# Kernel tuning notes

Measured on AMD Instinct MI355X. Metric: run time of the kernel, lower is better.

Reference implementation:

```python
import jax, jax.numpy as jnp
import numpy as np

DT = 1.0
COLL_COEF = 0.5  # module in training mode
TWO_PI = 2.0 * np.pi


def safe_norm_ch(d):
    # L2 norm over channel axis (axis=1) with torch-like zero-safe gradient
    sq = jnp.sum(d * d, axis=1)
    nz = sq > 0
    return jnp.sqrt(jnp.where(nz, sq, 1.0)) * nz


def setup_inputs() -> dict:
    key = jax.random.key(0)
    k1, k2, k3, k4 = jax.random.split(key, 4)
    bs, C, X = 4, 256, 1024
    kinet_dim = 128
    n = kinet_dim  # n_divide = max_channal // C = 1
    P = n * (n - 1) // 2  # 8128
    return {
        "x": jax.random.normal(k1, (bs, C, X), jnp.float32),
        "v": jax.random.normal(k2, (bs, C, X), jnp.float32),
        "a": jax.random.normal(k3, (bs, C, X), jnp.float32),
        "rand_u": jax.random.uniform(k4, (bs, C, P), jnp.float32),
        "collision_dims": jnp.arange(kinet_dim, dtype=jnp.int32),
    }


def reference(x, v, a, rand_u, collision_dims):
    dims = collision_dims
    xs = x[:, :, dims]          # (bs, chnl, n)  (n_divide == 1, view is a no-op)
    as_ = a[:, :, dims]
    bs, chnl, n = xs.shape
    vv = as_ * DT               # code overwrites v with a*dt
    xx = xs

    # pairwise relative / center-of-mass quantities
    x_r = safe_norm_ch(xx[:, :, :, None] - xx[:, :, None, :])       # (bs, n, n)
    v_r = safe_norm_ch(vv[:, :, :, None] - vv[:, :, None, :])       # (bs, n, n)
    v_cm = (vv[:, :, :, None] + vv[:, :, None, :]) * 0.5            # (bs, chnl, n, n)
    x_cm = (xx[:, :, :, None] + xx[:, :, None, :]) * 0.5            # (bs, chnl, n, n)

    u_x = jnp.exp(-x_r)
    v_r_max = jnp.max(v_r, axis=(1, 2), keepdims=True)              # (bs, 1, 1)
    mask = v_r / v_r_max * u_x
    collision_mask = mask > (1.0 - COLL_COEF)                       # (bs, n, n) bool

    # antisymmetric projection of the upper triangle of v_r
    iu, ju = np.triu_indices(n, k=1)
    rand_vec = TWO_PI * rand_u                                      # (bs, chnl, P)
    proj = v_r[:, iu, ju][:, None, :] * rand_vec                    # (bs, chnl, P)
    vrl = jnp.zeros((bs, chnl, n, n), xs.dtype)
    vrl = vrl.at[:, :, iu, ju].set(proj)
    vrl = vrl.at[:, :, ju, iu].set(-proj)

    delta_v = v_cm + vrl - vv[:, :, :, None]                        # (bs, chnl, n, n)
    cmask = collision_mask[:, None, :, :]
    v_new = vv + jnp.sum(delta_v * cmask, axis=2)                   # (bs, chnl, n)

    cm = collision_mask.astype(xs.dtype) + jnp.eye(n, dtype=xs.dtype)[None]
    x_new = jnp.sum(x_cm * cm[:, None], axis=2) / jnp.sum(cm, axis=2)[:, None, :]
    x_new = x_new + v_new * (DT / 2.0)

    # reassemble: zero collision dims of x and a, add, write back updated coords
    out = x.at[:, :, dims].set(0.0) + a.at[:, :, dims].set(0.0)
    out = out.at[:, :, dims].set(x_new.reshape(bs, chnl, n))
    return out
```

## Files before the change

### kernel.cpp

```cpp
#include <hip/hip_runtime.h>
#include <math.h>

#define BS 4
#define CH 256
#define XD 1024
#define N 128
#define NP 8128
#define TWO_PI_F 6.283185307179586f
#define PADU 132

typedef __fp16 h2v __attribute__((ext_vector_type(2)));

__device__ __forceinline__ h2v u2h(unsigned u) {
  union { unsigned u; h2v h; } x; x.u = u; return x.h;
}
__device__ __forceinline__ unsigned h2u(h2v h) {
  union { unsigned u; h2v h; } x; x.h = h; return x.u;
}

__global__ __launch_bounds__(256) void k1_pair_pass(
    const float* __restrict__ x, const float* __restrict__ a,
    const int* __restrict__ dims,
    float* __restrict__ vrS, float* __restrict__ mS,
    float* __restrict__ pmaxV, float* __restrict__ pmaxM,
    float* __restrict__ out) {
  int ti = blockIdx.x, tj = blockIdx.y, b = blockIdx.z;
  int t = threadIdx.x;
  __shared__ unsigned sXi[16][PADU], sXj[16][PADU], sAi[16][PADU], sAj[16][PADU];
  __shared__ unsigned inset[XD / 32];
  __shared__ float wred[16];

  if (t < XD / 32) inset[t] = 0u;
  __syncthreads();
  int d16 = t & 15, grp = t >> 4;
  int di, dj;
  if (t < N) atomicOr(&inset[dims[t] >> 5], 1u << (dims[t] & 31));
  di = dims[ti * 16 + d16];
  dj = dims[tj * 16 + d16];
  __syncthreads();

  {
    int B = (b << 6) + (tj << 3) + ti;
    int row = (B << 2) + (t >> 6);
    int q0 = t & 63;
    const float4* x4 = (const float4*)(x + (size_t)row * XD);
    const float4* a4 = (const float4*)(a + (size_t)row * XD);
    float4* o4 = (float4*)(out + (size_t)row * XD);
#pragma unroll
    for (int q = 0; q < 4; ++q) {
      int e = q0 + (q << 6);
      unsigned nib = (inset[e >> 3] >> ((e & 7) * 4)) & 0xFu;
      float4 xv = x4[e], av = a4[e];
      float4 o;
      o.x = fmaf((nib & 1u) ? 0.5f : 1.0f, av.x, xv.x);
      o.y = fmaf((nib & 2u) ? 0.5f : 1.0f, av.y, xv.y);
      o.z = fmaf((nib & 4u) ? 0.5f : 1.0f, av.z, xv.z);
      o.w = fmaf((nib & 8u) ? 0.5f : 1.0f, av.w, xv.w);
      o4[e] = o;
    }
  }

  {
    const float* xb = x + (size_t)b * CH * XD;
    const float* ab = a + (size_t)b * CH * XD;
    int c0 = grp * 16;
#pragma unroll
    for (int s = 0; s < 4; ++s) {
      const float* src = (s & 1) ? ab : xb;
      int d = (s & 2) ? dj : di;
      unsigned pk[8];
#pragma unroll
      for (int k = 0; k < 8; ++k) {
        float f0 = src[(size_t)(c0 + 2 * k) * XD + d];
        float f1 = src[(size_t)(c0 + 2 * k + 1) * XD + d];
        pk[k] = h2u(__builtin_amdgcn_cvt_pkrtz(f0, f1));
      }
      unsigned* dst = (s & 2) ? ((s & 1) ? &sAj[d16][0] : &sXj[d16][0])
                              : ((s & 1) ? &sAi[d16][0] : &sXi[d16][0]);
      *(uint4*)&dst[grp * 8] = make_uint4(pk[0], pk[1], pk[2], pk[3]);
      *(uint4*)&dst[grp * 8 + 4] = make_uint4(pk[4], pk[5], pk[6], pk[7]);
    }
  }
  __syncthreads();

  int ii = t >> 4, jj = t & 15;
  float accx = 0.f, accv = 0.f;
#pragma unroll 8
  for (int cq = 0; cq < 32; ++cq) {
    uint4 xi = *(const uint4*)&sXi[ii][cq * 4];
    uint4 xj = *(const uint4*)&sXj[jj][cq * 4];
    uint4 ai = *(const uint4*)&sAi[ii][cq * 4];
    uint4 aj = *(const uint4*)&sAj[jj][cq * 4];
    h2v d0 = u2h(xi.x) - u2h(xj.x);
    accx = __builtin_amdgcn_fdot2(d0, d0, accx, false);
    h2v d1 = u2h(xi.y) - u2h(xj.y);
    accx = __builtin_amdgcn_fdot2(d1, d1, accx, false);
    h2v d2 = u2h(xi.z) - u2h(xj.z);
    accx = __builtin_amdgcn_fdot2(d2, d2, accx, false);
    h2v d3 = u2h(xi.w) - u2h(xj.w);
    accx = __builtin_amdgcn_fdot2(d3, d3, accx, false);
    h2v e0 = u2h(ai.x) - u2h(aj.x);
    accv = __builtin_amdgcn_fdot2(e0, e0, accv, false);
    h2v e1 = u2h(ai.y) - u2h(aj.y);
    accv = __builtin_amdgcn_fdot2(e1, e1, accv, false);
    h2v e2 = u2h(ai.z) - u2h(aj.z);
    accv = __builtin_amdgcn_fdot2(e2, e2, accv, false);
    h2v e3 = u2h(ai.w) - u2h(aj.w);
    accv = __builtin_amdgcn_fdot2(e3, e3, accv, false);
  }
  float vr = sqrtf(accv);
  float mv = vr * expf(-sqrtf(accx));
  int i = ti * 16 + ii, j = tj * 16 + jj;
  vrS[((size_t)b * N + i) * N + j] = vr;
  mS[((size_t)b * N + i) * N + j] = mv;

  float wv = vr, wm = mv;
#pragma unroll
  for (int off = 32; off; off >>= 1) {
    wv = fmaxf(wv, __shfl_xor(wv, off));
    wm = fmaxf(wm, __shfl_xor(wm, off));
  }
  int wid = t >> 6;
  if ((t & 63) == 0) { wred[wid] = wv; wred[8 + wid] = wm; }
  __syncthreads();
  if (t == 0) {
    int tile = (b << 6) + (ti << 3) + tj;
    pmaxV[tile] = fmaxf(fmaxf(wred[0], wred[1]), fmaxf(wred[2], wred[3]));
    pmaxM[tile] = fmaxf(fmaxf(wred[8], wred[9]), fmaxf(wred[10], wred[11]));
  }
}

__global__ __launch_bounds__(256) void k2_fixup(
    const float* __restrict__ x, const float* __restrict__ a,
    const float* __restrict__ ru, const int* __restrict__ dims,
    const float* __restrict__ vrS, const float* __restrict__ mS,
    const float* __restrict__ pmaxV, const float* __restrict__ pmaxM,
    float* __restrict__ out) {
  int cg = blockIdx.x, b = blockIdx.y;
  int t = threadIdx.x;
  __shared__ float mx2[2];
  __shared__ float xx[N], vv[N];
  __shared__ int dsh[N];

  if (t < 64) {
    float pv = pmaxV[(b << 6) + t];
    float pm = pmaxM[(b << 6) + t];
#pragma unroll
    for (int off = 32; off; off >>= 1) {
      pv = fmaxf(pv, __shfl_xor(pv, off));
      pm = fmaxf(pm, __shfl_xor(pm, off));
    }
    if (t == 0) { mx2[0] = pv; mx2[1] = pm; }
  }
  __syncthreads();
  float vrmax = mx2[0], mmax = mx2[1];
  float inv = vrmax > 0.f ? 1.f / vrmax : 0.f;
  if (!(mmax * inv > 0.5f)) return;

  if (t < N) dsh[t] = dims[t];
  for (int cc = 0; cc < 32; ++cc) {
    int c = (cg << 5) + cc;
    int bc = (b << 8) + c;
    __syncthreads();
    if (t < N) {
      int d = dsh[t];
      xx[t] = x[(size_t)bc * XD + d];
      vv[t] = a[(size_t)bc * XD + d];
    }
    __syncthreads();
    if (t < N) {
      int j = t;
      const float* mcol = mS + (size_t)b * N * N + j;
      const float* vcol = vrS + (size_t)b * N * N + j;
      const float* rub = ru + (size_t)bc * NP;
      float S = 0.f, sumV = 0.f, sumX = 0.f, R = 0.f;
      for (int i = 0; i < N; ++i) {
        float mv = mcol[(size_t)i * N];
        if (mv * inv > 0.5f) {
          S += 1.f;
          sumV += vv[i];
          sumX += xx[i];
          float vrv = vcol[(size_t)i * N];
          int p;
          float sgn;
          if (i < j) {
            p = i * N - ((i * (i + 1)) >> 1) + (j - i - 1);
            sgn = 1.f;
          } else {
            p = j * N - ((j * (j + 1)) >> 1) + (i - j - 1);
            sgn = -1.f;
          }
          R += sgn * TWO_PI_F * vrv * rub[p];
        }
      }
      float vj = vv[j];
      float v_new = vj + 0.5f * S * vj - 0.5f * sumV + R;
      float x_new = 0.5f * xx[j] + 0.5f * (xx[j] + sumX) / (S + 1.f) + 0.5f * v_new;
      out[(size_t)bc * XD + dsh[j]] = x_new;
    }
  }
}

extern "C" void kernel_launch(void* const* d_in, const int* in_sizes, int n_in,
                              void* d_out, int out_size, void* d_ws, size_t ws_size,
                              hipStream_t stream) {
  const float* x = (const float*)d_in[0];
  const float* a = (const float*)d_in[2];
  const float* ru = (const float*)d_in[3];
  const int* dims = (const int*)d_in[4];
  float* out = (float*)d_out;

  float* vrS = (float*)d_ws;
  float* mS = vrS + (size_t)BS * N * N;
  float* pmaxV = mS + (size_t)BS * N * N;
  float* pmaxM = pmaxV + BS * 64;

  k1_pair_pass<<<dim3(8, 8, BS), 256, 0, stream>>>(x, a, dims, vrS, mS, pmaxV,
                                                   pmaxM, out);
  k2_fixup<<<dim3(8, BS), 256, 0, stream>>>(x, a, ru, dims, vrS, mS, pmaxV,
                                            pmaxM, out);
}
```

Measured before the change: 12.80 us.

## Widen pair-pass blocks to 1024 threads with split-channel partial sums

Each pair-pass block grows from 256 to 1024 threads. The streaming copy, the strided gather of the four channel tiles, and the channel dot-product loop are each split four ways across the extra threads. The channel partial sums are reduced through new shared-memory arrays before the sqrt/exp and max reduction, which adds a barrier. The aim is more memory-level parallelism and latency hiding for a small 256-block grid, at the cost of more shared memory and synchronisation per block.

```diff
diff --git a/kernel.cpp b/kernel.cpp
--- a/kernel.cpp
+++ b/kernel.cpp
@@ -18,7 +18,7 @@
   union { unsigned u; h2v h; } x; x.h = h; return x.u;
 }
 
-__global__ __launch_bounds__(256) void k1_pair_pass(
+__global__ __launch_bounds__(1024, 4) void k1_pair_pass(
     const float* __restrict__ x, const float* __restrict__ a,
     const int* __restrict__ dims,
     float* __restrict__ vrS, float* __restrict__ mS,
@@ -27,101 +27,105 @@
   int ti = blockIdx.x, tj = blockIdx.y, b = blockIdx.z;
   int t = threadIdx.x;
   __shared__ unsigned sXi[16][PADU], sXj[16][PADU], sAi[16][PADU], sAj[16][PADU];
+  __shared__ float paccX[4][256], paccV[4][256];
   __shared__ unsigned inset[XD / 32];
   __shared__ float wred[16];
 
   if (t < XD / 32) inset[t] = 0u;
   __syncthreads();
-  int d16 = t & 15, grp = t >> 4;
-  int di, dj;
   if (t < N) atomicOr(&inset[dims[t] >> 5], 1u << (dims[t] & 31));
-  di = dims[ti * 16 + d16];
-  dj = dims[tj * 16 + d16];
   __syncthreads();
 
   {
     int B = (b << 6) + (tj << 3) + ti;
-    int row = (B << 2) + (t >> 6);
-    int q0 = t & 63;
+    int row = (B << 2) + (t >> 8);
+    int e = t & 255;
     const float4* x4 = (const float4*)(x + (size_t)row * XD);
     const float4* a4 = (const float4*)(a + (size_t)row * XD);
     float4* o4 = (float4*)(out + (size_t)row * XD);
-#pragma unroll
-    for (int q = 0; q < 4; ++q) {
-      int e = q0 + (q << 6);
-      unsigned nib = (inset[e >> 3] >> ((e & 7) * 4)) & 0xFu;
-      float4 xv = x4[e], av = a4[e];
-      float4 o;
-      o.x = fmaf((nib & 1u) ? 0.5f : 1.0f, av.x, xv.x);
-      o.y = fmaf((nib & 2u) ? 0.5f : 1.0f, av.y, xv.y);
-      o.z = fmaf((nib & 4u) ? 0.5f : 1.0f, av.z, xv.z);
-      o.w = fmaf((nib & 8u) ? 0.5f : 1.0f, av.w, xv.w);
-      o4[e] = o;
-    }
+    unsigned nib = (inset[e >> 3] >> ((e & 7) * 4)) & 0xFu;
+    float4 xv = x4[e], av = a4[e];
+    float4 o;
+    o.x = fmaf((nib & 1u) ? 0.5f : 1.0f, av.x, xv.x);
+    o.y = fmaf((nib & 2u) ? 0.5f : 1.0f, av.y, xv.y);
+    o.z = fmaf((nib & 4u) ? 0.5f : 1.0f, av.z, xv.z);
+    o.w = fmaf((nib & 8u) ? 0.5f : 1.0f, av.w, xv.w);
+    o4[e] = o;
   }
 
   {
-    const float* xb = x + (size_t)b * CH * XD;
-    const float* ab = a + (size_t)b * CH * XD;
+    int s = t >> 8, r = t & 255;
+    int d16 = r & 15, grp = r >> 4;
     int c0 = grp * 16;
-#pragma unroll
-    for (int s = 0; s < 4; ++s) {
-      const float* src = (s & 1) ? ab : xb;
-      int d = (s & 2) ? dj : di;
-      unsigned pk[8];
-#pragma unroll
-      for (int k = 0; k < 8; ++k) {
-        float f0 = src[(size_t)(c0 + 2 * k) * XD + d];
-        float f1 = src[(size_t)(c0 + 2 * k + 1) * XD + d];
-        pk[k] = h2u(__builtin_amdgcn_cvt_pkrtz(f0, f1));
-      }
-      unsigned* dst = (s & 2) ? ((s & 1) ? &sAj[d16][0] : &sXj[d16][0])
-                              : ((s & 1) ? &sAi[d16][0] : &sXi[d16][0]);
-      *(uint4*)&dst[grp * 8] = make_uint4(pk[0], pk[1], pk[2], pk[3]);
-      *(uint4*)&dst[grp * 8 + 4] = make_uint4(pk[4], pk[5], pk[6], pk[7]);
-    }
-  }
-  __syncthreads();
-
-  int ii = t >> 4, jj = t & 15;
-  float accx = 0.f, accv = 0.f;
-#pragma unroll 8
-  for (int cq = 0; cq < 32; ++cq) {
-    uint4 xi = *(const uint4*)&sXi[ii][cq * 4];
-    uint4 xj = *(const uint4*)&sXj[jj][cq * 4];
-    uint4 ai = *(const uint4*)&sAi[ii][cq * 4];
-    uint4 aj = *(const uint4*)&sAj[jj][cq * 4];
-    h2v d0 = u2h(xi.x) - u2h(xj.x);
-    accx = __builtin_amdgcn_fdot2(d0, d0, accx, false);
-    h2v d1 = u2h(xi.y) - u2h(xj.y);
-    accx = __builtin_amdgcn_fdot2(d1, d1, accx, false);
-    h2v d2 = u2h(xi.z) - u2h(xj.z);
-    accx = __builtin_amdgcn_fdot2(d2, d2, accx, false);
-    h2v d3 = u2h(xi.w) - u2h(xj.w);
-    accx = __builtin_amdgcn_fdot2(d3, d3, accx, false);
-    h2v e0 = u2h(ai.x) - u2h(aj.x);
-    accv = __builtin_amdgcn_fdot2(e0, e0, accv, false);
-    h2v e1 = u2h(ai.y) - u2h(aj.y);
-    accv = __builtin_amdgcn_fdot2(e1, e1, accv, false);
-    h2v e2 = u2h(ai.z) - u2h(aj.z);
-    accv = __builtin_amdgcn_fdot2(e2, e2, accv, false);
-    h2v e3 = u2h(ai.w) - u2h(aj.w);
-    accv = __builtin_amdgcn_fdot2(e3, e3, accv, false);
-  }
-  float vr = sqrtf(accv);
-  float mv = vr * expf(-sqrtf(accx));
-  int i = ti * 16 + ii, j = tj * 16 + jj;
-  vrS[((size_t)b * N + i) * N + j] = vr;
-  mS[((size_t)b * N + i) * N + j] = mv;
-
-  float wv = vr, wm = mv;
-#pragma unroll
-  for (int off = 32; off; off >>= 1) {
-    wv = fmaxf(wv, __shfl_xor(wv, off));
-    wm = fmaxf(wm, __shfl_xor(wm, off));
-  }
-  int wid = t >> 6;
-  if ((t & 63) == 0) { wred[wid] = wv; wred[8 + wid] = wm; }
+    int d = dims[((s & 1) ? tj : ti) * 16 + d16];
+    const float* src = ((s >= 2) ? a : x) + (size_t)b * CH * XD;
+    unsigned pk[8];
+#pragma unroll
+    for (int k = 0; k < 8; ++k) {
+      float f0 = src[(size_t)(c0 + 2 * k) * XD + d];
+      float f1 = src[(size_t)(c0 + 2 * k + 1) * XD + d];
+      pk[k] = h2u(__builtin_amdgcn_cvt_pkrtz(f0, f1));
+    }
+    unsigned* dst = (s == 0) ? &sXi[d16][0]
+                  : (s == 1) ? &sXj[d16][0]
+                  : (s == 2) ? &sAi[d16][0]
+                             : &sAj[d16][0];
+    *(uint4*)&dst[grp * 8] = make_uint4(pk[0], pk[1], pk[2], pk[3]);
+    *(uint4*)&dst[grp * 8 + 4] = make_uint4(pk[4], pk[5], pk[6], pk[7]);
+  }
+  __syncthreads();
+
+  {
+    int p = t & 255, q = t >> 8;
+    int ii = p >> 4, jj = p & 15;
+    int u0 = q * 32;
+    float accx = 0.f, accv = 0.f;
+#pragma unroll
+    for (int cq = 0; cq < 8; ++cq) {
+      uint4 xi = *(const uint4*)&sXi[ii][u0 + cq * 4];
+      uint4 xj = *(const uint4*)&sXj[jj][u0 + cq * 4];
+      uint4 ai = *(const uint4*)&sAi[ii][u0 + cq * 4];
+      uint4 aj = *(const uint4*)&sAj[jj][u0 + cq * 4];
+      h2v d0 = u2h(xi.x) - u2h(xj.x);
+      accx = __builtin_amdgcn_fdot2(d0, d0, accx, false);
+      h2v d1 = u2h(xi.y) - u2h(xj.y);
+      accx = __builtin_amdgcn_fdot2(d1, d1, accx, false);
+      h2v d2 = u2h(xi.z) - u2h(xj.z);
+      accx = __builtin_amdgcn_fdot2(d2, d2, accx, false);
+      h2v d3 = u2h(xi.w) - u2h(xj.w);
+      accx = __builtin_amdgcn_fdot2(d3, d3, accx, false);
+      h2v e0 = u2h(ai.x) - u2h(aj.x);
+      accv = __builtin_amdgcn_fdot2(e0, e0, accv, false);
+      h2v e1 = u2h(ai.y) - u2h(aj.y);
+      accv = __builtin_amdgcn_fdot2(e1, e1, accv, false);
+      h2v e2 = u2h(ai.z) - u2h(aj.z);
+      accv = __builtin_amdgcn_fdot2(e2, e2, accv, false);
+      h2v e3 = u2h(ai.w) - u2h(aj.w);
+      accv = __builtin_amdgcn_fdot2(e3, e3, accv, false);
+    }
+    paccX[q][p] = accx;
+    paccV[q][p] = accv;
+  }
+  __syncthreads();
+
+  if (t < 256) {
+    float accx = paccX[0][t] + paccX[1][t] + paccX[2][t] + paccX[3][t];
+    float accv = paccV[0][t] + paccV[1][t] + paccV[2][t] + paccV[3][t];
+    float vr = sqrtf(accv);
+    float mv = vr * expf(-sqrtf(accx));
+    int i = ti * 16 + (t >> 4), j = tj * 16 + (t & 15);
+    vrS[((size_t)b * N + i) * N + j] = vr;
+    mS[((size_t)b * N + i) * N + j] = mv;
+
+    float wv = vr, wm = mv;
+#pragma unroll
+    for (int off = 32; off; off >>= 1) {
+      wv = fmaxf(wv, __shfl_xor(wv, off));
+      wm = fmaxf(wm, __shfl_xor(wm, off));
+    }
+    int wid = t >> 6;
+    if ((t & 63) == 0) { wred[wid] = wv; wred[8 + wid] = wm; }
+  }
   __syncthreads();
   if (t == 0) {
     int tile = (b << 6) + (ti << 3) + tj;
@@ -215,8 +219,8 @@
   float* pmaxV = mS + (size_t)BS * N * N;
   float* pmaxM = pmaxV + BS * 64;
 
-  k1_pair_pass<<<dim3(8, 8, BS), 256, 0, stream>>>(x, a, dims, vrS, mS, pmaxV,
-                                                   pmaxM, out);
+  k1_pair_pass<<<dim3(8, 8, BS), 1024, 0, stream>>>(x, a, dims, vrS, mS, pmaxV,
+                                                    pmaxM, out);
   k2_fixup<<<dim3(8, BS), 256, 0, stream>>>(x, a, ru, dims, vrS, mS, pmaxV,
                                             pmaxM, out);
 }
```

New measurement: 13.77 us. 1.08x slower.

## Fuse pair pass and fixup into one kernel via last-block atomic counter

Applied to the files above, without the earlier changes.

Merges the two kernels into one launch. Each block publishes its partial maxima and bumps a per-batch atomic counter, and the last block to arrive for a batch runs the collision fixup. This removes a kernel launch and the gap between launches. In exchange, when collisions occur the fixup for all 256 channels runs in a single block per batch, down from eight blocks, which serialises that work. The counter relies on modulo-64 wraparound across calls, so the workspace must start at zero.

```diff
diff --git a/kernel.cpp b/kernel.cpp
--- a/kernel.cpp
+++ b/kernel.cpp
@@ -18,25 +18,27 @@
   union { unsigned u; h2v h; } x; x.h = h; return x.u;
 }
 
-__global__ __launch_bounds__(256) void k1_pair_pass(
+__global__ __launch_bounds__(256) void k_fused(
     const float* __restrict__ x, const float* __restrict__ a,
-    const int* __restrict__ dims,
+    const float* __restrict__ ru, const int* __restrict__ dims,
     float* __restrict__ vrS, float* __restrict__ mS,
     float* __restrict__ pmaxV, float* __restrict__ pmaxM,
-    float* __restrict__ out) {
+    unsigned* __restrict__ cnt, float* __restrict__ out) {
   int ti = blockIdx.x, tj = blockIdx.y, b = blockIdx.z;
   int t = threadIdx.x;
   __shared__ unsigned sXi[16][PADU], sXj[16][PADU], sAi[16][PADU], sAj[16][PADU];
   __shared__ unsigned inset[XD / 32];
   __shared__ float wred[16];
+  __shared__ int islast;
+  __shared__ float mx2[2];
+  __shared__ float xx[N], vv[N];
 
   if (t < XD / 32) inset[t] = 0u;
   __syncthreads();
   int d16 = t & 15, grp = t >> 4;
-  int di, dj;
   if (t < N) atomicOr(&inset[dims[t] >> 5], 1u << (dims[t] & 31));
-  di = dims[ti * 16 + d16];
-  dj = dims[tj * 16 + d16];
+  int di = dims[ti * 16 + d16];
+  int dj = dims[tj * 16 + d16];
   __syncthreads();
 
   {
@@ -110,9 +112,13 @@
   }
   float vr = sqrtf(accv);
   float mv = vr * expf(-sqrtf(accx));
-  int i = ti * 16 + ii, j = tj * 16 + jj;
-  vrS[((size_t)b * N + i) * N + j] = vr;
-  mS[((size_t)b * N + i) * N + j] = mv;
+  {
+    int i = ti * 16 + ii, j = tj * 16 + jj;
+    __hip_atomic_store(&vrS[((size_t)b * N + i) * N + j], vr, __ATOMIC_RELAXED,
+                       __HIP_MEMORY_SCOPE_AGENT);
+    __hip_atomic_store(&mS[((size_t)b * N + i) * N + j], mv, __ATOMIC_RELAXED,
+                       __HIP_MEMORY_SCOPE_AGENT);
+  }
 
   float wv = vr, wm = mv;
 #pragma unroll
@@ -125,26 +131,25 @@
   __syncthreads();
   if (t == 0) {
     int tile = (b << 6) + (ti << 3) + tj;
-    pmaxV[tile] = fmaxf(fmaxf(wred[0], wred[1]), fmaxf(wred[2], wred[3]));
-    pmaxM[tile] = fmaxf(fmaxf(wred[8], wred[9]), fmaxf(wred[10], wred[11]));
-  }
-}
-
-__global__ __launch_bounds__(256) void k2_fixup(
-    const float* __restrict__ x, const float* __restrict__ a,
-    const float* __restrict__ ru, const int* __restrict__ dims,
-    const float* __restrict__ vrS, const float* __restrict__ mS,
-    const float* __restrict__ pmaxV, const float* __restrict__ pmaxM,
-    float* __restrict__ out) {
-  int cg = blockIdx.x, b = blockIdx.y;
-  int t = threadIdx.x;
-  __shared__ float mx2[2];
-  __shared__ float xx[N], vv[N];
-  __shared__ int dsh[N];
+    __hip_atomic_store(&pmaxV[tile],
+                       fmaxf(fmaxf(wred[0], wred[1]), fmaxf(wred[2], wred[3])),
+                       __ATOMIC_RELAXED, __HIP_MEMORY_SCOPE_AGENT);
+    __hip_atomic_store(&pmaxM[tile],
+                       fmaxf(fmaxf(wred[8], wred[9]), fmaxf(wred[10], wred[11])),
+                       __ATOMIC_RELAXED, __HIP_MEMORY_SCOPE_AGENT);
+    __threadfence();
+    unsigned old = __hip_atomic_fetch_add(&cnt[b], 1u, __ATOMIC_ACQ_REL,
+                                          __HIP_MEMORY_SCOPE_AGENT);
+    islast = ((old & 63u) == 63u);
+  }
+  __syncthreads();
+  if (!islast) return;
 
   if (t < 64) {
-    float pv = pmaxV[(b << 6) + t];
-    float pm = pmaxM[(b << 6) + t];
+    float pv = __hip_atomic_load(&pmaxV[(b << 6) + t], __ATOMIC_RELAXED,
+                                 __HIP_MEMORY_SCOPE_AGENT);
+    float pm = __hip_atomic_load(&pmaxM[(b << 6) + t], __ATOMIC_RELAXED,
+                                 __HIP_MEMORY_SCOPE_AGENT);
 #pragma unroll
     for (int off = 32; off; off >>= 1) {
       pv = fmaxf(pv, __shfl_xor(pv, off));
@@ -157,13 +162,11 @@
   float inv = vrmax > 0.f ? 1.f / vrmax : 0.f;
   if (!(mmax * inv > 0.5f)) return;
 
-  if (t < N) dsh[t] = dims[t];
-  for (int cc = 0; cc < 32; ++cc) {
-    int c = (cg << 5) + cc;
+  for (int c = 0; c < CH; ++c) {
     int bc = (b << 8) + c;
     __syncthreads();
     if (t < N) {
-      int d = dsh[t];
+      int d = dims[t];
       xx[t] = x[(size_t)bc * XD + d];
       vv[t] = a[(size_t)bc * XD + d];
     }
@@ -175,12 +178,14 @@
       const float* rub = ru + (size_t)bc * NP;
       float S = 0.f, sumV = 0.f, sumX = 0.f, R = 0.f;
       for (int i = 0; i < N; ++i) {
-        float mv = mcol[(size_t)i * N];
-        if (mv * inv > 0.5f) {
+        float mvv = __hip_atomic_load(&mcol[(size_t)i * N], __ATOMIC_RELAXED,
+                                      __HIP_MEMORY_SCOPE_AGENT);
+        if (mvv * inv > 0.5f) {
           S += 1.f;
           sumV += vv[i];
           sumX += xx[i];
-          float vrv = vcol[(size_t)i * N];
+          float vrv = __hip_atomic_load(&vcol[(size_t)i * N], __ATOMIC_RELAXED,
+                                        __HIP_MEMORY_SCOPE_AGENT);
           int p;
           float sgn;
           if (i < j) {
@@ -196,7 +201,7 @@
       float vj = vv[j];
       float v_new = vj + 0.5f * S * vj - 0.5f * sumV + R;
       float x_new = 0.5f * xx[j] + 0.5f * (xx[j] + sumX) / (S + 1.f) + 0.5f * v_new;
-      out[(size_t)bc * XD + dsh[j]] = x_new;
+      out[(size_t)bc * XD + dims[j]] = x_new;
     }
   }
 }
@@ -214,9 +219,8 @@
   float* mS = vrS + (size_t)BS * N * N;
   float* pmaxV = mS + (size_t)BS * N * N;
   float* pmaxM = pmaxV + BS * 64;
-
-  k1_pair_pass<<<dim3(8, 8, BS), 256, 0, stream>>>(x, a, dims, vrS, mS, pmaxV,
-                                                   pmaxM, out);
-  k2_fixup<<<dim3(8, BS), 256, 0, stream>>>(x, a, ru, dims, vrS, mS, pmaxV,
-                                            pmaxM, out);
-}
+  unsigned* cnt = (unsigned*)(pmaxM + BS * 64);
+
+  k_fused<<<dim3(8, 8, BS), 256, 0, stream>>>(x, a, ru, dims, vrS, mS, pmaxV,
+                                              pmaxM, cnt, out);
+}
```

Result: slower. 18.30 us (+43.0%).

## Compute only upper-triangle pair tiles and split passthrough copy into separate blocks

Applied to the files above, without the earlier changes.

The pair kernel now launches only the 36 upper-triangular 16x16 tiles per batch instead of all 64, using the symmetry of the pairwise norms. The fixup kernel reads the mask and v_r through min/max indices, so it still sees the full matrix. The bulk x+a passthrough copy moves out of the pair blocks into 112 dedicated blocks with row ranges, so copy and compute run in separate blocks. The risks are a less coalesced lo/hi access pattern in the fixup loop and a serial while loop to decode the tile index.

```diff
diff --git a/kernel.cpp b/kernel.cpp
--- a/kernel.cpp
+++ b/kernel.cpp
@@ -6,6 +6,8 @@
 #define XD 1024
 #define N 128
 #define NP 8128
+#define NTILE 36
+#define NPASS 112
 #define TWO_PI_F 6.283185307179586f
 #define PADU 132
 
@@ -24,43 +26,21 @@
     float* __restrict__ vrS, float* __restrict__ mS,
     float* __restrict__ pmaxV, float* __restrict__ pmaxM,
     float* __restrict__ out) {
-  int ti = blockIdx.x, tj = blockIdx.y, b = blockIdx.z;
+  int bid = blockIdx.x;
   int t = threadIdx.x;
   __shared__ unsigned sXi[16][PADU], sXj[16][PADU], sAi[16][PADU], sAj[16][PADU];
   __shared__ unsigned inset[XD / 32];
   __shared__ float wred[16];
 
-  if (t < XD / 32) inset[t] = 0u;
-  __syncthreads();
-  int d16 = t & 15, grp = t >> 4;
-  int di, dj;
-  if (t < N) atomicOr(&inset[dims[t] >> 5], 1u << (dims[t] & 31));
-  di = dims[ti * 16 + d16];
-  dj = dims[tj * 16 + d16];
-  __syncthreads();
-
-  {
-    int B = (b << 6) + (tj << 3) + ti;
-    int row = (B << 2) + (t >> 6);
-    int q0 = t & 63;
-    const float4* x4 = (const float4*)(x + (size_t)row * XD);
-    const float4* a4 = (const float4*)(a + (size_t)row * XD);
-    float4* o4 = (float4*)(out + (size_t)row * XD);
-#pragma unroll
-    for (int q = 0; q < 4; ++q) {
-      int e = q0 + (q << 6);
-      unsigned nib = (inset[e >> 3] >> ((e & 7) * 4)) & 0xFu;
-      float4 xv = x4[e], av = a4[e];
-      float4 o;
-      o.x = fmaf((nib & 1u) ? 0.5f : 1.0f, av.x, xv.x);
-      o.y = fmaf((nib & 2u) ? 0.5f : 1.0f, av.y, xv.y);
-      o.z = fmaf((nib & 4u) ? 0.5f : 1.0f, av.z, xv.z);
-      o.w = fmaf((nib & 8u) ? 0.5f : 1.0f, av.w, xv.w);
-      o4[e] = o;
-    }
-  }
-
-  {
+  if (bid < BS * NTILE) {
+    int b = bid / NTILE, tt = bid % NTILE;
+    int ti = 0;
+    while (8 * (ti + 1) - ((ti + 1) * ti) / 2 <= tt) ++ti;
+    int tj = ti + tt - (8 * ti - (ti * (ti - 1)) / 2);
+
+    int d16 = t & 15, grp = t >> 4;
+    int di = dims[ti * 16 + d16];
+    int dj = dims[tj * 16 + d16];
     const float* xb = x + (size_t)b * CH * XD;
     const float* ab = a + (size_t)b * CH * XD;
     int c0 = grp * 16;
@@ -80,53 +60,74 @@
       *(uint4*)&dst[grp * 8] = make_uint4(pk[0], pk[1], pk[2], pk[3]);
       *(uint4*)&dst[grp * 8 + 4] = make_uint4(pk[4], pk[5], pk[6], pk[7]);
     }
-  }
-  __syncthreads();
-
-  int ii = t >> 4, jj = t & 15;
-  float accx = 0.f, accv = 0.f;
+    __syncthreads();
+
+    int ii = t >> 4, jj = t & 15;
+    float accx = 0.f, accv = 0.f;
 #pragma unroll 8
-  for (int cq = 0; cq < 32; ++cq) {
-    uint4 xi = *(const uint4*)&sXi[ii][cq * 4];
-    uint4 xj = *(const uint4*)&sXj[jj][cq * 4];
-    uint4 ai = *(const uint4*)&sAi[ii][cq * 4];
-    uint4 aj = *(const uint4*)&sAj[jj][cq * 4];
-    h2v d0 = u2h(xi.x) - u2h(xj.x);
-    accx = __builtin_amdgcn_fdot2(d0, d0, accx, false);
-    h2v d1 = u2h(xi.y) - u2h(xj.y);
-    accx = __builtin_amdgcn_fdot2(d1, d1, accx, false);
-    h2v d2 = u2h(xi.z) - u2h(xj.z);
-    accx = __builtin_amdgcn_fdot2(d2, d2, accx, false);
-    h2v d3 = u2h(xi.w) - u2h(xj.w);
-    accx = __builtin_amdgcn_fdot2(d3, d3, accx, false);
-    h2v e0 = u2h(ai.x) - u2h(aj.x);
-    accv = __builtin_amdgcn_fdot2(e0, e0, accv, false);
-    h2v e1 = u2h(ai.y) - u2h(aj.y);
-    accv = __builtin_amdgcn_fdot2(e1, e1, accv, false);
-    h2v e2 = u2h(ai.z) - u2h(aj.z);
-    accv = __builtin_amdgcn_fdot2(e2, e2, accv, false);
-    h2v e3 = u2h(ai.w) - u2h(aj.w);
-    accv = __builtin_amdgcn_fdot2(e3, e3, accv, false);
-  }
-  float vr = sqrtf(accv);
-  float mv = vr * expf(-sqrtf(accx));
-  int i = ti * 16 + ii, j = tj * 16 + jj;
-  vrS[((size_t)b * N + i) * N + j] = vr;
-  mS[((size_t)b * N + i) * N + j] = mv;
-
-  float wv = vr, wm = mv;
-#pragma unroll
-  for (int off = 32; off; off >>= 1) {
-    wv = fmaxf(wv, __shfl_xor(wv, off));
-    wm = fmaxf(wm, __shfl_xor(wm, off));
-  }
-  int wid = t >> 6;
-  if ((t & 63) == 0) { wred[wid] = wv; wred[8 + wid] = wm; }
-  __syncthreads();
-  if (t == 0) {
-    int tile = (b << 6) + (ti << 3) + tj;
-    pmaxV[tile] = fmaxf(fmaxf(wred[0], wred[1]), fmaxf(wred[2], wred[3]));
-    pmaxM[tile] = fmaxf(fmaxf(wred[8], wred[9]), fmaxf(wred[10], wred[11]));
+    for (int cq = 0; cq < 32; ++cq) {
+      uint4 xi = *(const uint4*)&sXi[ii][cq * 4];
+      uint4 xj = *(const uint4*)&sXj[jj][cq * 4];
+      uint4 ai = *(const uint4*)&sAi[ii][cq * 4];
+      uint4 aj = *(const uint4*)&sAj[jj][cq * 4];
+      h2v d0 = u2h(xi.x) - u2h(xj.x);
+      accx = __builtin_amdgcn_fdot2(d0, d0, accx, false);
+      h2v d1 = u2h(xi.y) - u2h(xj.y);
+      accx = __builtin_amdgcn_fdot2(d1, d1, accx, false);
+      h2v d2 = u2h(xi.z) - u2h(xj.z);
+      accx = __builtin_amdgcn_fdot2(d2, d2, accx, false);
+      h2v d3 = u2h(xi.w) - u2h(xj.w);
+      accx = __builtin_amdgcn_fdot2(d3, d3, accx, false);
+      h2v e0 = u2h(ai.x) - u2h(aj.x);
+      accv = __builtin_amdgcn_fdot2(e0, e0, accv, false);
+      h2v e1 = u2h(ai.y) - u2h(aj.y);
+      accv = __builtin_amdgcn_fdot2(e1, e1, accv, false);
+      h2v e2 = u2h(ai.z) - u2h(aj.z);
+      accv = __builtin_amdgcn_fdot2(e2, e2, accv, false);
+      h2v e3 = u2h(ai.w) - u2h(aj.w);
+      accv = __builtin_amdgcn_fdot2(e3, e3, accv, false);
+    }
+    float vr = sqrtf(accv);
+    float mv = vr * expf(-sqrtf(accx));
+    int i = ti * 16 + ii, j = tj * 16 + jj;
+    vrS[((size_t)b * N + i) * N + j] = vr;
+    mS[((size_t)b * N + i) * N + j] = mv;
+
+    float wv = vr, wm = mv;
+#pragma unroll
+    for (int off = 32; off; off >>= 1) {
+      wv = fmaxf(wv, __shfl_xor(wv, off));
+      wm = fmaxf(wm, __shfl_xor(wm, off));
+    }
+    int wid = t >> 6;
+    if ((t & 63) == 0) { wred[wid] = wv; wred[8 + wid] = wm; }
+    __syncthreads();
+    if (t == 0) {
+      pmaxV[b * NTILE + tt] = fmaxf(fmaxf(wred[0], wred[1]), fmaxf(wred[2], wred[3]));
+      pmaxM[b * NTILE + tt] = fmaxf(fmaxf(wred[8], wred[9]), fmaxf(wred[10], wred[11]));
+    }
+  } else {
+    int pb = bid - BS * NTILE;
+    if (t < XD / 32) inset[t] = 0u;
+    __syncthreads();
+    if (t < N) atomicOr(&inset[dims[t] >> 5], 1u << (dims[t] & 31));
+    __syncthreads();
+    int r0 = (pb * (BS * CH)) / NPASS;
+    int r1 = ((pb + 1) * (BS * CH)) / NPASS;
+    for (int row = r0; row < r1; ++row) {
+      const float4* x4 = (const float4*)(x + (size_t)row * XD);
+      const float4* a4 = (const float4*)(a + (size_t)row * XD);
+      float4* o4 = (float4*)(out + (size_t)row * XD);
+      int e = t;
+      unsigned nib = (inset[e >> 3] >> ((e & 7) * 4)) & 0xFu;
+      float4 xv = x4[e], av = a4[e];
+      float4 o;
+      o.x = fmaf((nib & 1u) ? 0.5f : 1.0f, av.x, xv.x);
+      o.y = fmaf((nib & 2u) ? 0.5f : 1.0f, av.y, xv.y);
+      o.z = fmaf((nib & 4u) ? 0.5f : 1.0f, av.z, xv.z);
+      o.w = fmaf((nib & 8u) ? 0.5f : 1.0f, av.w, xv.w);
+      o4[e] = o;
+    }
   }
 }
 
@@ -143,8 +144,8 @@
   __shared__ int dsh[N];
 
   if (t < 64) {
-    float pv = pmaxV[(b << 6) + t];
-    float pm = pmaxM[(b << 6) + t];
+    float pv = (t < NTILE) ? pmaxV[b * NTILE + t] : 0.f;
+    float pm = (t < NTILE) ? pmaxM[b * NTILE + t] : 0.f;
 #pragma unroll
     for (int off = 32; off; off >>= 1) {
       pv = fmaxf(pv, __shfl_xor(pv, off));
@@ -170,17 +171,17 @@
     __syncthreads();
     if (t < N) {
       int j = t;
-      const float* mcol = mS + (size_t)b * N * N + j;
-      const float* vcol = vrS + (size_t)b * N * N + j;
       const float* rub = ru + (size_t)bc * NP;
       float S = 0.f, sumV = 0.f, sumX = 0.f, R = 0.f;
       for (int i = 0; i < N; ++i) {
-        float mv = mcol[(size_t)i * N];
-        if (mv * inv > 0.5f) {
+        int lo = i < j ? i : j, hi = i < j ? j : i;
+        size_t idx = ((size_t)b * N + lo) * N + hi;
+        float mvv = mS[idx];
+        if (mvv * inv > 0.5f) {
           S += 1.f;
           sumV += vv[i];
           sumX += xx[i];
-          float vrv = vcol[(size_t)i * N];
+          float vrv = vrS[idx];
           int p;
           float sgn;
           if (i < j) {
@@ -213,10 +214,10 @@
   float* vrS = (float*)d_ws;
   float* mS = vrS + (size_t)BS * N * N;
   float* pmaxV = mS + (size_t)BS * N * N;
-  float* pmaxM = pmaxV + BS * 64;
-
-  k1_pair_pass<<<dim3(8, 8, BS), 256, 0, stream>>>(x, a, dims, vrS, mS, pmaxV,
-                                                   pmaxM, out);
+  float* pmaxM = pmaxV + BS * NTILE;
+
+  k1_pair_pass<<<BS * NTILE + NPASS, 256, 0, stream>>>(x, a, dims, vrS, mS,
+                                                       pmaxV, pmaxM, out);
   k2_fixup<<<dim3(8, BS), 256, 0, stream>>>(x, a, ru, dims, vrS, mS, pmaxV,
                                             pmaxM, out);
 }
```

New measurement: 11.85 us, median of 2. -7.4%, faster.
